# Kernel tuning notes

Measured on AMD Instinct MI355X. Metric: run time of the kernel, lower is better.

The kernel has to match this reference:

```python
import jax, jax.numpy as jnp
import numpy as np

B, N, E = 128, 2048, 32768   # events, nodes per history graph, temporal edges per graph
C, TC, H = 4, 4, 2           # channels, time_channels, heads (hardcoded in source)
DH = C // H
L = 2                        # num_layers


def setup_inputs() -> dict:
    key = jax.random.key(0)
    ks = jax.random.split(key, 16)
    return {
        "x": jax.random.normal(ks[0], (B, N, C), jnp.float32),
        "edge_index": jax.random.randint(ks[1], (B, 2, E), 0, N),
        "edge_time": jax.random.uniform(ks[2], (B, E), jnp.float32),
        "timestamp": jax.random.uniform(ks[3], (B,), jnp.float32),
        "src_index": jax.random.randint(ks[4], (B,), 0, N),
        "dst_index": jax.random.randint(ks[5], (B,), 0, N),
        "time_w": jax.random.normal(ks[6], (TC,), jnp.float32),
        "time_b": jax.random.normal(ks[7], (TC,), jnp.float32),
        "Wq": jax.random.normal(ks[8], (L, C, C), jnp.float32) / np.sqrt(C).astype(np.float32),
        "Wk": jax.random.normal(ks[9], (L, C + TC, C), jnp.float32) / np.sqrt(C + TC).astype(np.float32),
        "Wv": jax.random.normal(ks[10], (L, C + TC, C), jnp.float32) / np.sqrt(C + TC).astype(np.float32),
        "Wo": jax.random.normal(ks[11], (L, C, C), jnp.float32) / np.sqrt(C).astype(np.float32),
        "bo": jnp.zeros((L, C), jnp.float32),
        "W_lin": jax.random.normal(ks[12], (2 * C + TC, 2), jnp.float32) / np.sqrt(2 * C + TC).astype(np.float32),
        "b_lin": jnp.zeros((2,), jnp.float32),
    }


def _time_enc(t, w, b):
    # TimeEncoder: cos(t * w + b)  (Bochner-style functional time encoding)
    return jnp.cos(t[..., None] * w + b)


def _encode(x, src, dst, phi, Wq, Wk, Wv, Wo, bo):
    # seg id per edge: (batch, dst node) -> flat segment for segment softmax
    seg = (jnp.arange(B, dtype=dst.dtype)[:, None] * N + dst).reshape(-1)  # [B*E]
    h = x
    for l in range(L):
        h_src = jnp.take_along_axis(h, src[:, :, None], axis=1)            # [B,E,C] gather source feats
        msg = jnp.concatenate([h_src, phi], axis=-1)                       # [B,E,C+TC]
        q = (h @ Wq[l]).reshape(B, N, C)                                   # [B,N,C]
        k = (msg @ Wk[l]).reshape(B, E, H, DH)
        v = (msg @ Wv[l]).reshape(B, E, H, DH)
        q_e = jnp.take_along_axis(q, dst[:, :, None], axis=1).reshape(B, E, H, DH)
        logits = (q_e * k).sum(-1) / np.float32(np.sqrt(DH))               # [B,E,H]
        lf = logits.reshape(B * E, H)
        m = jax.ops.segment_max(lf, seg, num_segments=B * N)               # stable softmax max
        p = jnp.exp(lf - m[seg])
        s = jax.ops.segment_sum(p, seg, num_segments=B * N)
        agg = jax.ops.segment_sum(p[:, :, None] * v.reshape(B * E, H, DH), seg, num_segments=B * N)
        attn = (agg / jnp.where(s == 0, 1.0, s)[:, :, None]).reshape(B, N, C)
        h = jax.nn.relu(h + attn @ Wo[l] + bo[l])                          # residual + out-proj + relu
    return h


def reference(x, edge_index, edge_time, timestamp, src_index, dst_index,
              time_w, time_b, Wq, Wk, Wv, Wo, bo, W_lin, b_lin):
    src, dst = edge_index[:, 0, :], edge_index[:, 1, :]
    dt = timestamp[:, None] - edge_time                                    # [B,E] time deltas vs query time
    phi = _time_enc(dt, time_w, time_b)                                    # [B,E,TC]
    h = _encode(x, src, dst, phi, Wq, Wk, Wv, Wo, bo)                      # [B,N,C]
    bidx = jnp.arange(B)
    src_x = h[bidx, src_index]                                             # [B,C]
    dst_x = h[bidx, dst_index]                                             # [B,C]
    time_x = _time_enc(timestamp, time_w, time_b)                          # [B,TC]
    feats = jnp.concatenate([src_x, dst_x, time_x], axis=-1)               # [B,12]
    return feats @ W_lin + b_lin                                           # [B,2]
```

## Files before the change

### kernel.cpp

```cpp
#include <hip/hip_runtime.h>

namespace {

constexpr int B = 128, N = 2048, E = 32768;
constexpr int LOG2N = 11, LOG2E = 15;
constexpr int QE = E / 4;
constexpr int LOG2QE = 13;

constexpr size_t OFF_H0 = 0;
constexpr size_t OFF_H1 = 4u * 1024 * 1024;
constexpr size_t OFF_S8 = 8u * 1024 * 1024;
constexpr size_t OFF_RP = 40u * 1024 * 1024;

__global__ __launch_bounds__(1024) void sort_kernel(const int* __restrict__ edge_index,
                                                    const float* __restrict__ edge_time,
                                                    const float* __restrict__ timestamp,
                                                    int2* __restrict__ sorted8,
                                                    int* __restrict__ row_ptr) {
  __shared__ int  cnt[N];
  __shared__ int  wsum[16];
  __shared__ int2 rec[QE];
  int blk = blockIdx.x, b = blk >> 2, q = blk & 3, t = threadIdx.x;

  cnt[t] = 0; cnt[t + 1024] = 0;
  __syncthreads();

  const int* src_arr = edge_index + (((size_t)(2 * b)) << LOG2E) + q * QE;
  const int* dst_arr = edge_index + (((size_t)(2 * b + 1)) << LOG2E) + q * QE;
  const float* et    = edge_time + (((size_t)b) << LOG2E) + q * QE;
  float ts = timestamp[b];

  int srcv[8], dstv[8]; float dtv[8];
#pragma unroll
  for (int k = 0; k < 8; ++k) {
    int e = t + k * 1024;
    srcv[k] = src_arr[e];
    dstv[k] = dst_arr[e];
    dtv[k]  = ts - et[e];
  }

#pragma unroll
  for (int k = 0; k < 8; ++k) atomicAdd(&cnt[dstv[k]], 1);
  __syncthreads();

  int i0 = 2 * t, i1 = 2 * t + 1;
  int l0 = cnt[i0], l1 = cnt[i1];
  int sum = l0 + l1;
  int lane = t & 63, wid = t >> 6;
  int incl = sum;
#pragma unroll
  for (int d = 1; d < 64; d <<= 1) {
    int v = __shfl_up(incl, d, 64);
    if (lane >= d) incl += v;
  }
  if (lane == 63) wsum[wid] = incl;
  __syncthreads();
  if (t < 16) {
    int v = wsum[t];
    int inc = v;
#pragma unroll
    for (int d = 1; d < 16; d <<= 1) {
      int u = __shfl_up(inc, d, 16);
      if (t >= d) inc += u;
    }
    wsum[t] = inc - v;
  }
  __syncthreads();
  int run = wsum[wid] + (incl - sum);
  int run2 = run + l0;
  int* rp = row_ptr + (size_t)blk * (N + 1);
  rp[i0] = run;
  rp[i1] = run2;
  if (t == 1023) rp[N] = QE;
  cnt[i0] = run;
  cnt[i1] = run2;
  __syncthreads();

#pragma unroll
  for (int k = 0; k < 8; ++k) {
    int pos = atomicAdd(&cnt[dstv[k]], 1);
    rec[pos] = make_int2(srcv[k], __float_as_int(dtv[k]));
  }
  __syncthreads();

  const int4* rec4 = (const int4*)rec;
  int4* out4 = (int4*)(sorted8 + (((size_t)blk) << LOG2QE));
#pragma unroll
  for (int i = t; i < QE / 2; i += 1024) out4[i] = rec4[i];
}

__global__ __launch_bounds__(1024) void layer_kernel(const float4* __restrict__ h_in,
                                                     float4* __restrict__ h_out,
                                                     const int* __restrict__ row_ptr,
                                                     const int2* __restrict__ sorted8,
                                                     const float* __restrict__ tw,
                                                     const float* __restrict__ tb,
                                                     const float* __restrict__ Wq,
                                                     const float* __restrict__ Wk,
                                                     const float* __restrict__ Wv,
                                                     const float* __restrict__ Wo,
                                                     const float* __restrict__ bo) {
  __shared__ float4 lh[N];
  int blk = blockIdx.x, b = blk >> 1, half = blk & 1, t = threadIdx.x;

  const float4* hb = h_in + (((size_t)b) << LOG2N);
  lh[t] = hb[t];
  lh[t + 1024] = hb[t + 1024];

  constexpr float INV2PI = 0.15915494309189535f;
  constexpr float QSCALE = 0.70710678118654752f * 1.4426950408889634f;
  float twf2[4], tbf2[4], wq[16], wkh[16], wkp[16], wvh[16], wvp[16];
#pragma unroll
  for (int j = 0; j < 4; j++) { twf2[j] = tw[j] * INV2PI; tbf2[j] = tb[j] * INV2PI; }
#pragma unroll
  for (int j = 0; j < 16; j++) wq[j] = Wq[j];
#pragma unroll
  for (int j = 0; j < 16; j++) { wkh[j] = Wk[j]; wkp[j] = Wk[16 + j]; }
#pragma unroll
  for (int j = 0; j < 16; j++) { wvh[j] = Wv[j]; wvp[j] = Wv[16 + j]; }
  __syncthreads();

  int n = half * 1024 + t;
  {
    float4 hn = lh[n];
    float q0 = (hn.x * wq[0] + hn.y * wq[4] + hn.z * wq[8]  + hn.w * wq[12]) * QSCALE;
    float q1 = (hn.x * wq[1] + hn.y * wq[5] + hn.z * wq[9]  + hn.w * wq[13]) * QSCALE;
    float q2 = (hn.x * wq[2] + hn.y * wq[6] + hn.z * wq[10] + hn.w * wq[14]) * QSCALE;
    float q3 = (hn.x * wq[3] + hn.y * wq[7] + hn.z * wq[11] + hn.w * wq[15]) * QSCALE;
#pragma unroll
    for (int i = 0; i < 4; i++) {
      wq[i]      = q0 * wkh[i * 4 + 0] + q1 * wkh[i * 4 + 1];
      wq[4 + i]  = q2 * wkh[i * 4 + 2] + q3 * wkh[i * 4 + 3];
      wq[8 + i]  = q0 * wkp[i * 4 + 0] + q1 * wkp[i * 4 + 1];
      wq[12 + i] = q2 * wkp[i * 4 + 2] + q3 * wkp[i * 4 + 3];
    }
  }

  int stage = 0, addr, rem, total;
  int b1, b2, b3, c1, c2, c3;
  {
    const int* rp0 = row_ptr + (size_t)(b * 4 + 0) * (N + 1);
    const int* rp1 = row_ptr + (size_t)(b * 4 + 1) * (N + 1);
    const int* rp2 = row_ptr + (size_t)(b * 4 + 2) * (N + 1);
    const int* rp3 = row_ptr + (size_t)(b * 4 + 3) * (N + 1);
    int s0 = rp0[n], e0 = rp0[n + 1];
    int s1 = rp1[n], e1 = rp1[n + 1];
    int s2 = rp2[n], e2 = rp2[n + 1];
    int s3 = rp3[n], e3 = rp3[n + 1];
    int c0 = e0 - s0; c1 = e1 - s1; c2 = e2 - s2; c3 = e3 - s3;
    total = c0 + c1 + c2 + c3;
    addr = ((b * 4 + 0) << LOG2QE) + s0; rem = c0;
    b1 = ((b * 4 + 1) << LOG2QE) + s1;
    b2 = ((b * 4 + 2) << LOG2QE) + s2;
    b3 = ((b * 4 + 3) << LOG2QE) + s3;
    while (rem <= 0 && stage < 3) {
      ++stage;
      addr = (stage == 1) ? b1 : (stage == 2) ? b2 : b3;
      rem  = (stage == 1) ? c1 : (stage == 2) ? c2 : c3;
    }
  }

#define ADV() do { ++addr; --rem;                                   \
    while (rem <= 0 && stage < 3) { ++stage;                        \
      addr = (stage == 1) ? b1 : (stage == 2) ? b2 : b3;            \
      rem  = (stage == 1) ? c1 : (stage == 2) ? c2 : c3; } } while (0)
#define HW_COS(d, s) asm("v_cos_f32 %0, %1" : "=v"(d) : "v"(s))
#define HW_EXP2(d, s) asm("v_exp_f32 %0, %1" : "=v"(d) : "v"(s))

  float s0v = 0.f, s1v = 0.f, a00 = 0.f, a01 = 0.f, a10 = 0.f, a11 = 0.f;

  int2 r0 = sorted8[addr]; ADV();
  int2 r1 = sorted8[addr]; ADV();
  int2 r2 = sorted8[addr]; ADV();
  int2 r3 = sorted8[addr]; ADV();
  float4 hsN = lh[r0.x & (N - 1)];

  for (int it = 0; it < total; ++it) {
    int2 cur = r0;
    float4 hs = hsN;
    r0 = r1; r1 = r2; r2 = r3;
    r3 = sorted8[addr]; ADV();
    hsN = lh[r0.x & (N - 1)];

    float dt = __int_as_float(cur.y);
    float ph0, ph1, ph2, ph3;
    HW_COS(ph0, dt * twf2[0] + tbf2[0]);
    HW_COS(ph1, dt * twf2[1] + tbf2[1]);
    HW_COS(ph2, dt * twf2[2] + tbf2[2]);
    HW_COS(ph3, dt * twf2[3] + tbf2[3]);

    float l0 = hs.x * wq[0] + hs.y * wq[1] + hs.z * wq[2]  + hs.w * wq[3]
             + ph0 * wq[8] + ph1 * wq[9] + ph2 * wq[10] + ph3 * wq[11];
    float l1 = hs.x * wq[4] + hs.y * wq[5] + hs.z * wq[6]  + hs.w * wq[7]
             + ph0 * wq[12] + ph1 * wq[13] + ph2 * wq[14] + ph3 * wq[15];

    float p0, p1;
    HW_EXP2(p0, l0);
    HW_EXP2(p1, l1);

    float v0 = hs.x * wvh[0] + hs.y * wvh[4] + hs.z * wvh[8]  + hs.w * wvh[12]
             + ph0 * wvp[0] + ph1 * wvp[4] + ph2 * wvp[8]  + ph3 * wvp[12];
    float v1 = hs.x * wvh[1] + hs.y * wvh[5] + hs.z * wvh[9]  + hs.w * wvh[13]
             + ph0 * wvp[1] + ph1 * wvp[5] + ph2 * wvp[9]  + ph3 * wvp[13];
    float v2 = hs.x * wvh[2] + hs.y * wvh[6] + hs.z * wvh[10] + hs.w * wvh[14]
             + ph0 * wvp[2] + ph1 * wvp[6] + ph2 * wvp[10] + ph3 * wvp[14];
    float v3 = hs.x * wvh[3] + hs.y * wvh[7] + hs.z * wvh[11] + hs.w * wvh[15]
             + ph0 * wvp[3] + ph1 * wvp[7] + ph2 * wvp[11] + ph3 * wvp[15];

    s0v += p0; a00 += p0 * v0; a01 += p0 * v1;
    s1v += p1; a10 += p1 * v2; a11 += p1 * v3;
  }
#undef ADV
#undef HW_COS
#undef HW_EXP2

  float den0 = (s0v == 0.f) ? 1.f : s0v;
  float den1 = (s1v == 0.f) ? 1.f : s1v;
  float at0 = a00 / den0, at1 = a01 / den0, at2 = a10 / den1, at3 = a11 / den1;

  float wof[16], bof[4];
#pragma unroll
  for (int j = 0; j < 16; j++) wof[j] = Wo[j];
#pragma unroll
  for (int j = 0; j < 4; j++) bof[j] = bo[j];

  float4 hn = lh[n];
  float o0 = bof[0] + at0 * wof[0] + at1 * wof[4] + at2 * wof[8]  + at3 * wof[12];
  float o1 = bof[1] + at0 * wof[1] + at1 * wof[5] + at2 * wof[9]  + at3 * wof[13];
  float o2 = bof[2] + at0 * wof[2] + at1 * wof[6] + at2 * wof[10] + at3 * wof[14];
  float o3 = bof[3] + at0 * wof[3] + at1 * wof[7] + at2 * wof[11] + at3 * wof[15];
  h_out[(((size_t)b) << LOG2N) + n] =
      make_float4(fmaxf(hn.x + o0, 0.f), fmaxf(hn.y + o1, 0.f),
                  fmaxf(hn.z + o2, 0.f), fmaxf(hn.w + o3, 0.f));
}

__global__ void final_kernel(const float4* __restrict__ h,
                             const int* __restrict__ src_index, const int* __restrict__ dst_index,
                             const float* __restrict__ timestamp,
                             const float* __restrict__ tw,
                             const float* __restrict__ tb,
                             const float* __restrict__ W_lin,
                             const float* __restrict__ b_lin,
                             float* __restrict__ out) {
  int b = threadIdx.x;
  if (b >= B) return;
  float4 sx = h[(((size_t)b) << LOG2N) + src_index[b]];
  float4 dx = h[(((size_t)b) << LOG2N) + dst_index[b]];
  float ts = timestamp[b];
  float f[12];
  f[0] = sx.x; f[1] = sx.y; f[2] = sx.z; f[3] = sx.w;
  f[4] = dx.x; f[5] = dx.y; f[6] = dx.z; f[7] = dx.w;
#pragma unroll
  for (int j = 0; j < 4; j++) f[8 + j] = __cosf(ts * tw[j] + tb[j]);
#pragma unroll
  for (int c = 0; c < 2; c++) {
    float o = b_lin[c];
#pragma unroll
    for (int j = 0; j < 12; j++) o += f[j] * W_lin[j * 2 + c];
    out[b * 2 + c] = o;
  }
}

}

extern "C" void kernel_launch(void* const* d_in, const int* in_sizes, int n_in,
                              void* d_out, int out_size, void* d_ws, size_t ws_size,
                              hipStream_t stream) {
  (void)in_sizes; (void)n_in; (void)out_size; (void)ws_size;
  const float* x         = (const float*)d_in[0];
  const int*   edge_idx  = (const int*)d_in[1];
  const float* edge_time = (const float*)d_in[2];
  const float* timestamp = (const float*)d_in[3];
  const int*   src_index = (const int*)d_in[4];
  const int*   dst_index = (const int*)d_in[5];
  const float* time_w    = (const float*)d_in[6];
  const float* time_b    = (const float*)d_in[7];
  const float* Wq        = (const float*)d_in[8];
  const float* Wk        = (const float*)d_in[9];
  const float* Wv        = (const float*)d_in[10];
  const float* Wo        = (const float*)d_in[11];
  const float* bo        = (const float*)d_in[12];
  const float* W_lin     = (const float*)d_in[13];
  const float* b_lin     = (const float*)d_in[14];

  char* ws = (char*)d_ws;
  float4* h0      = (float4*)(ws + OFF_H0);
  float4* h1      = (float4*)(ws + OFF_H1);
  int2*   sorted8 = (int2*)(ws + OFF_S8);
  int*    row_ptr = (int*)(ws + OFF_RP);

  sort_kernel<<<4 * B, 1024, 0, stream>>>(edge_idx, edge_time, timestamp, sorted8, row_ptr);

  layer_kernel<<<2 * B, 1024, 0, stream>>>((const float4*)x, h1, row_ptr, sorted8,
                                           time_w, time_b,
                                           Wq + 0 * 16, Wk + 0 * 32, Wv + 0 * 32,
                                           Wo + 0 * 16, bo + 0 * 4);
  layer_kernel<<<2 * B, 1024, 0, stream>>>(h1, h0, row_ptr, sorted8,
                                           time_w, time_b,
                                           Wq + 1 * 16, Wk + 1 * 32, Wv + 1 * 32,
                                           Wo + 1 * 16, bo + 1 * 4);

  final_kernel<<<1, 128, 0, stream>>>(h0, src_index, dst_index, timestamp, time_w, time_b,
                                      W_lin, b_lin, (float*)d_out);
}
```

Measured before the change: 166.7 us.

## Fuse sort, both layers and final head into one cooperative persistent kernel

Replaces four kernel launches with a single cooperative kernel of 256 blocks that sort, run both attention layers and compute the final linear head, separated by grid-wide syncs. Each block sorts two edge quarters, then reuses its row-pointer loads across both layers. Blocks are mapped so a batch's blocks share an XCD for L2 locality. It removes launch gaps and redundant row_ptr reads, but adds grid-sync overhead and halves sort parallelism, since each block now does two quarters serially.

```diff
diff --git a/kernel.cpp b/kernel.cpp
--- a/kernel.cpp
+++ b/kernel.cpp
@@ -1,4 +1,7 @@
 #include <hip/hip_runtime.h>
+#include <hip/hip_cooperative_groups.h>
+
+namespace cg = cooperative_groups;
 
 namespace {
 
@@ -12,101 +15,50 @@
 constexpr size_t OFF_S8 = 8u * 1024 * 1024;
 constexpr size_t OFF_RP = 40u * 1024 * 1024;
 
-__global__ __launch_bounds__(1024) void sort_kernel(const int* __restrict__ edge_index,
-                                                    const float* __restrict__ edge_time,
-                                                    const float* __restrict__ timestamp,
-                                                    int2* __restrict__ sorted8,
-                                                    int* __restrict__ row_ptr) {
-  __shared__ int  cnt[N];
-  __shared__ int  wsum[16];
-  __shared__ int2 rec[QE];
-  int blk = blockIdx.x, b = blk >> 2, q = blk & 3, t = threadIdx.x;
-
-  cnt[t] = 0; cnt[t + 1024] = 0;
-  __syncthreads();
-
-  const int* src_arr = edge_index + (((size_t)(2 * b)) << LOG2E) + q * QE;
-  const int* dst_arr = edge_index + (((size_t)(2 * b + 1)) << LOG2E) + q * QE;
-  const float* et    = edge_time + (((size_t)b) << LOG2E) + q * QE;
-  float ts = timestamp[b];
-
-  int srcv[8], dstv[8]; float dtv[8];
-#pragma unroll
-  for (int k = 0; k < 8; ++k) {
-    int e = t + k * 1024;
-    srcv[k] = src_arr[e];
-    dstv[k] = dst_arr[e];
-    dtv[k]  = ts - et[e];
-  }
-
-#pragma unroll
-  for (int k = 0; k < 8; ++k) atomicAdd(&cnt[dstv[k]], 1);
-  __syncthreads();
-
-  int i0 = 2 * t, i1 = 2 * t + 1;
-  int l0 = cnt[i0], l1 = cnt[i1];
-  int sum = l0 + l1;
-  int lane = t & 63, wid = t >> 6;
-  int incl = sum;
-#pragma unroll
-  for (int d = 1; d < 64; d <<= 1) {
-    int v = __shfl_up(incl, d, 64);
-    if (lane >= d) incl += v;
-  }
-  if (lane == 63) wsum[wid] = incl;
-  __syncthreads();
-  if (t < 16) {
-    int v = wsum[t];
-    int inc = v;
-#pragma unroll
-    for (int d = 1; d < 16; d <<= 1) {
-      int u = __shfl_up(inc, d, 16);
-      if (t >= d) inc += u;
-    }
-    wsum[t] = inc - v;
-  }
-  __syncthreads();
-  int run = wsum[wid] + (incl - sum);
-  int run2 = run + l0;
-  int* rp = row_ptr + (size_t)blk * (N + 1);
-  rp[i0] = run;
-  rp[i1] = run2;
-  if (t == 1023) rp[N] = QE;
-  cnt[i0] = run;
-  cnt[i1] = run2;
-  __syncthreads();
-
-#pragma unroll
-  for (int k = 0; k < 8; ++k) {
-    int pos = atomicAdd(&cnt[dstv[k]], 1);
-    rec[pos] = make_int2(srcv[k], __float_as_int(dtv[k]));
-  }
-  __syncthreads();
-
-  const int4* rec4 = (const int4*)rec;
-  int4* out4 = (int4*)(sorted8 + (((size_t)blk) << LOG2QE));
-#pragma unroll
-  for (int i = t; i < QE / 2; i += 1024) out4[i] = rec4[i];
-}
-
-__global__ __launch_bounds__(1024) void layer_kernel(const float4* __restrict__ h_in,
-                                                     float4* __restrict__ h_out,
-                                                     const int* __restrict__ row_ptr,
-                                                     const int2* __restrict__ sorted8,
-                                                     const float* __restrict__ tw,
-                                                     const float* __restrict__ tb,
-                                                     const float* __restrict__ Wq,
-                                                     const float* __restrict__ Wk,
-                                                     const float* __restrict__ Wv,
-                                                     const float* __restrict__ Wo,
-                                                     const float* __restrict__ bo) {
-  __shared__ float4 lh[N];
-  int blk = blockIdx.x, b = blk >> 1, half = blk & 1, t = threadIdx.x;
-
+struct Params {
+  const float4* x;
+  const int*    edge_index;
+  const float*  edge_time;
+  const float*  timestamp;
+  const int*    src_index;
+  const int*    dst_index;
+  const float*  tw;
+  const float*  tb;
+  const float*  Wq;
+  const float*  Wk;
+  const float*  Wv;
+  const float*  Wo;
+  const float*  bo;
+  const float*  W_lin;
+  const float*  b_lin;
+  float4* h0;
+  float4* h1;
+  int2*   sorted8;
+  int*    row_ptr;
+  float*  out;
+};
+
+__device__ __forceinline__ float hw_cos(float s)  { float d; asm("v_cos_f32 %0, %1" : "=v"(d) : "v"(s)); return d; }
+__device__ __forceinline__ float hw_exp2(float s) { float d; asm("v_exp_f32 %0, %1" : "=v"(d) : "v"(s)); return d; }
+
+struct SortS { int cnt[N]; int wsum[16]; int2 rec[QE]; };
+
+__device__ __forceinline__ void layer_phase(
+    const Params& P, int b, int n, int t, int l,
+    const float4* __restrict__ h_in, float4* __restrict__ h_out, float4* lh,
+    int s0, int s1, int s2, int s3, int c0, int c1, int c2, int c3) {
   const float4* hb = h_in + (((size_t)b) << LOG2N);
   lh[t] = hb[t];
   lh[t + 1024] = hb[t + 1024];
 
+  const float* tw = P.tw;
+  const float* tb = P.tb;
+  const float* Wq = P.Wq + l * 16;
+  const float* Wk = P.Wk + l * 32;
+  const float* Wv = P.Wv + l * 32;
+  const float* Wo = P.Wo + l * 16;
+  const float* bo = P.bo + l * 4;
+
   constexpr float INV2PI = 0.15915494309189535f;
   constexpr float QSCALE = 0.70710678118654752f * 1.4426950408889634f;
   float twf2[4], tbf2[4], wq[16], wkh[16], wkp[16], wvh[16], wvp[16];
@@ -120,7 +72,6 @@
   for (int j = 0; j < 16; j++) { wvh[j] = Wv[j]; wvp[j] = Wv[16 + j]; }
   __syncthreads();
 
-  int n = half * 1024 + t;
   {
     float4 hn = lh[n];
     float q0 = (hn.x * wq[0] + hn.y * wq[4] + hn.z * wq[8]  + hn.w * wq[12]) * QSCALE;
@@ -136,67 +87,52 @@
     }
   }
 
-  int stage = 0, addr, rem, total;
-  int b1, b2, b3, c1, c2, c3;
-  {
-    const int* rp0 = row_ptr + (size_t)(b * 4 + 0) * (N + 1);
-    const int* rp1 = row_ptr + (size_t)(b * 4 + 1) * (N + 1);
-    const int* rp2 = row_ptr + (size_t)(b * 4 + 2) * (N + 1);
-    const int* rp3 = row_ptr + (size_t)(b * 4 + 3) * (N + 1);
-    int s0 = rp0[n], e0 = rp0[n + 1];
-    int s1 = rp1[n], e1 = rp1[n + 1];
-    int s2 = rp2[n], e2 = rp2[n + 1];
-    int s3 = rp3[n], e3 = rp3[n + 1];
-    int c0 = e0 - s0; c1 = e1 - s1; c2 = e2 - s2; c3 = e3 - s3;
-    total = c0 + c1 + c2 + c3;
-    addr = ((b * 4 + 0) << LOG2QE) + s0; rem = c0;
-    b1 = ((b * 4 + 1) << LOG2QE) + s1;
-    b2 = ((b * 4 + 2) << LOG2QE) + s2;
-    b3 = ((b * 4 + 3) << LOG2QE) + s3;
-    while (rem <= 0 && stage < 3) {
-      ++stage;
-      addr = (stage == 1) ? b1 : (stage == 2) ? b2 : b3;
-      rem  = (stage == 1) ? c1 : (stage == 2) ? c2 : c3;
-    }
+  int stage = 0;
+  int total = c0 + c1 + c2 + c3;
+  int addr = ((b * 4 + 0) << LOG2QE) + s0, rem = c0;
+  int b1 = ((b * 4 + 1) << LOG2QE) + s1;
+  int b2 = ((b * 4 + 2) << LOG2QE) + s2;
+  int b3 = ((b * 4 + 3) << LOG2QE) + s3;
+  while (rem <= 0 && stage < 3) {
+    ++stage;
+    addr = (stage == 1) ? b1 : (stage == 2) ? b2 : b3;
+    rem  = (stage == 1) ? c1 : (stage == 2) ? c2 : c3;
   }
 
 #define ADV() do { ++addr; --rem;                                   \
     while (rem <= 0 && stage < 3) { ++stage;                        \
       addr = (stage == 1) ? b1 : (stage == 2) ? b2 : b3;            \
       rem  = (stage == 1) ? c1 : (stage == 2) ? c2 : c3; } } while (0)
-#define HW_COS(d, s) asm("v_cos_f32 %0, %1" : "=v"(d) : "v"(s))
-#define HW_EXP2(d, s) asm("v_exp_f32 %0, %1" : "=v"(d) : "v"(s))
 
   float s0v = 0.f, s1v = 0.f, a00 = 0.f, a01 = 0.f, a10 = 0.f, a11 = 0.f;
 
-  int2 r0 = sorted8[addr]; ADV();
-  int2 r1 = sorted8[addr]; ADV();
-  int2 r2 = sorted8[addr]; ADV();
-  int2 r3 = sorted8[addr]; ADV();
+  const int2* __restrict__ srt = P.sorted8;
+  int2 r0 = srt[addr]; ADV();
+  int2 r1 = srt[addr]; ADV();
+  int2 r2 = srt[addr]; ADV();
+  int2 r3 = srt[addr]; ADV();
   float4 hsN = lh[r0.x & (N - 1)];
 
   for (int it = 0; it < total; ++it) {
     int2 cur = r0;
     float4 hs = hsN;
     r0 = r1; r1 = r2; r2 = r3;
-    r3 = sorted8[addr]; ADV();
+    r3 = srt[addr]; ADV();
     hsN = lh[r0.x & (N - 1)];
 
     float dt = __int_as_float(cur.y);
-    float ph0, ph1, ph2, ph3;
-    HW_COS(ph0, dt * twf2[0] + tbf2[0]);
-    HW_COS(ph1, dt * twf2[1] + tbf2[1]);
-    HW_COS(ph2, dt * twf2[2] + tbf2[2]);
-    HW_COS(ph3, dt * twf2[3] + tbf2[3]);
+    float ph0 = hw_cos(dt * twf2[0] + tbf2[0]);
+    float ph1 = hw_cos(dt * twf2[1] + tbf2[1]);
+    float ph2 = hw_cos(dt * twf2[2] + tbf2[2]);
+    float ph3 = hw_cos(dt * twf2[3] + tbf2[3]);
 
     float l0 = hs.x * wq[0] + hs.y * wq[1] + hs.z * wq[2]  + hs.w * wq[3]
              + ph0 * wq[8] + ph1 * wq[9] + ph2 * wq[10] + ph3 * wq[11];
     float l1 = hs.x * wq[4] + hs.y * wq[5] + hs.z * wq[6]  + hs.w * wq[7]
              + ph0 * wq[12] + ph1 * wq[13] + ph2 * wq[14] + ph3 * wq[15];
 
-    float p0, p1;
-    HW_EXP2(p0, l0);
-    HW_EXP2(p1, l1);
+    float p0 = hw_exp2(l0);
+    float p1 = hw_exp2(l1);
 
     float v0 = hs.x * wvh[0] + hs.y * wvh[4] + hs.z * wvh[8]  + hs.w * wvh[12]
              + ph0 * wvp[0] + ph1 * wvp[4] + ph2 * wvp[8]  + ph3 * wvp[12];
@@ -211,8 +147,6 @@
     s1v += p1; a10 += p1 * v2; a11 += p1 * v3;
   }
 #undef ADV
-#undef HW_COS
-#undef HW_EXP2
 
   float den0 = (s0v == 0.f) ? 1.f : s0v;
   float den1 = (s1v == 0.f) ? 1.f : s1v;
@@ -234,30 +168,127 @@
                   fmaxf(hn.z + o2, 0.f), fmaxf(hn.w + o3, 0.f));
 }
 
-__global__ void final_kernel(const float4* __restrict__ h,
-                             const int* __restrict__ src_index, const int* __restrict__ dst_index,
-                             const float* __restrict__ timestamp,
-                             const float* __restrict__ tw,
-                             const float* __restrict__ tb,
-                             const float* __restrict__ W_lin,
-                             const float* __restrict__ b_lin,
-                             float* __restrict__ out) {
-  int b = threadIdx.x;
-  if (b >= B) return;
-  float4 sx = h[(((size_t)b) << LOG2N) + src_index[b]];
-  float4 dx = h[(((size_t)b) << LOG2N) + dst_index[b]];
-  float ts = timestamp[b];
-  float f[12];
-  f[0] = sx.x; f[1] = sx.y; f[2] = sx.z; f[3] = sx.w;
-  f[4] = dx.x; f[5] = dx.y; f[6] = dx.z; f[7] = dx.w;
-#pragma unroll
-  for (int j = 0; j < 4; j++) f[8 + j] = __cosf(ts * tw[j] + tb[j]);
-#pragma unroll
-  for (int c = 0; c < 2; c++) {
-    float o = b_lin[c];
-#pragma unroll
-    for (int j = 0; j < 12; j++) o += f[j] * W_lin[j * 2 + c];
-    out[b * 2 + c] = o;
+__global__ __launch_bounds__(1024) void fused_kernel(Params P) {
+  __shared__ __align__(16) char smem[sizeof(SortS)];
+  int p = blockIdx.x, t = threadIdx.x;
+  int xcd = p & 7, slot = p >> 3;
+  int b = xcd * 16 + (slot >> 1);
+  int half = slot & 1;
+
+  {
+    SortS& S = *reinterpret_cast<SortS*>(smem);
+    float ts = P.timestamp[b];
+    for (int qi = 0; qi < 2; ++qi) {
+      int q = 2 * half + qi;
+      int blk = b * 4 + q;
+      S.cnt[t] = 0; S.cnt[t + 1024] = 0;
+      __syncthreads();
+
+      const int* src_arr = P.edge_index + (((size_t)(2 * b)) << LOG2E) + q * QE;
+      const int* dst_arr = P.edge_index + (((size_t)(2 * b + 1)) << LOG2E) + q * QE;
+      const float* et    = P.edge_time + (((size_t)b) << LOG2E) + q * QE;
+
+      int srcv[8], dstv[8]; float dtv[8];
+#pragma unroll
+      for (int k = 0; k < 8; ++k) {
+        int e = t + k * 1024;
+        srcv[k] = src_arr[e];
+        dstv[k] = dst_arr[e];
+        dtv[k]  = ts - et[e];
+      }
+#pragma unroll
+      for (int k = 0; k < 8; ++k) atomicAdd(&S.cnt[dstv[k]], 1);
+      __syncthreads();
+
+      int i0 = 2 * t, i1 = 2 * t + 1;
+      int l0 = S.cnt[i0], l1 = S.cnt[i1];
+      int sum = l0 + l1;
+      int lane = t & 63, wid = t >> 6;
+      int incl = sum;
+#pragma unroll
+      for (int d = 1; d < 64; d <<= 1) {
+        int v = __shfl_up(incl, d, 64);
+        if (lane >= d) incl += v;
+      }
+      if (lane == 63) S.wsum[wid] = incl;
+      __syncthreads();
+      if (t < 16) {
+        int v = S.wsum[t];
+        int inc = v;
+#pragma unroll
+        for (int d = 1; d < 16; d <<= 1) {
+          int u = __shfl_up(inc, d, 16);
+          if (t >= d) inc += u;
+        }
+        S.wsum[t] = inc - v;
+      }
+      __syncthreads();
+      int run = S.wsum[wid] + (incl - sum);
+      int run2 = run + l0;
+      int* rp = P.row_ptr + (size_t)blk * (N + 1);
+      rp[i0] = run;
+      rp[i1] = run2;
+      if (t == 1023) rp[N] = QE;
+      S.cnt[i0] = run;
+      S.cnt[i1] = run2;
+      __syncthreads();
+
+#pragma unroll
+      for (int k = 0; k < 8; ++k) {
+        int pos = atomicAdd(&S.cnt[dstv[k]], 1);
+        S.rec[pos] = make_int2(srcv[k], __float_as_int(dtv[k]));
+      }
+      __syncthreads();
+
+      const int4* rec4 = (const int4*)S.rec;
+      int4* out4 = (int4*)(P.sorted8 + (((size_t)blk) << LOG2QE));
+      for (int i = t; i < QE / 2; i += 1024) out4[i] = rec4[i];
+      __syncthreads();
+    }
+  }
+  __threadfence();
+  cg::this_grid().sync();
+
+  int n = half * 1024 + t;
+  int s0, s1, s2, s3, c0, c1, c2, c3;
+  {
+    const int* rp0 = P.row_ptr + (size_t)(b * 4 + 0) * (N + 1);
+    const int* rp1 = P.row_ptr + (size_t)(b * 4 + 1) * (N + 1);
+    const int* rp2 = P.row_ptr + (size_t)(b * 4 + 2) * (N + 1);
+    const int* rp3 = P.row_ptr + (size_t)(b * 4 + 3) * (N + 1);
+    s0 = rp0[n]; c0 = rp0[n + 1] - s0;
+    s1 = rp1[n]; c1 = rp1[n + 1] - s1;
+    s2 = rp2[n]; c2 = rp2[n + 1] - s2;
+    s3 = rp3[n]; c3 = rp3[n + 1] - s3;
+  }
+
+  float4* lh = reinterpret_cast<float4*>(smem);
+
+  layer_phase(P, b, n, t, 0, P.x, P.h1, lh, s0, s1, s2, s3, c0, c1, c2, c3);
+  __threadfence();
+  cg::this_grid().sync();
+
+  layer_phase(P, b, n, t, 1, P.h1, P.h0, lh, s0, s1, s2, s3, c0, c1, c2, c3);
+  __threadfence();
+  cg::this_grid().sync();
+
+  if (p == 0 && t < B) {
+    int bb = t;
+    float4 sx = P.h0[(((size_t)bb) << LOG2N) + P.src_index[bb]];
+    float4 dx = P.h0[(((size_t)bb) << LOG2N) + P.dst_index[bb]];
+    float ts = P.timestamp[bb];
+    float f[12];
+    f[0] = sx.x; f[1] = sx.y; f[2] = sx.z; f[3] = sx.w;
+    f[4] = dx.x; f[5] = dx.y; f[6] = dx.z; f[7] = dx.w;
+#pragma unroll
+    for (int j = 0; j < 4; j++) f[8 + j] = __cosf(ts * P.tw[j] + P.tb[j]);
+#pragma unroll
+    for (int c = 0; c < 2; c++) {
+      float o = P.b_lin[c];
+#pragma unroll
+      for (int j = 0; j < 12; j++) o += f[j] * P.W_lin[j * 2 + c];
+      P.out[bb * 2 + c] = o;
+    }
   }
 }
 
@@ -267,39 +298,31 @@
                               void* d_out, int out_size, void* d_ws, size_t ws_size,
                               hipStream_t stream) {
   (void)in_sizes; (void)n_in; (void)out_size; (void)ws_size;
-  const float* x         = (const float*)d_in[0];
-  const int*   edge_idx  = (const int*)d_in[1];
-  const float* edge_time = (const float*)d_in[2];
-  const float* timestamp = (const float*)d_in[3];
-  const int*   src_index = (const int*)d_in[4];
-  const int*   dst_index = (const int*)d_in[5];
-  const float* time_w    = (const float*)d_in[6];
-  const float* time_b    = (const float*)d_in[7];
-  const float* Wq        = (const float*)d_in[8];
-  const float* Wk        = (const float*)d_in[9];
-  const float* Wv        = (const float*)d_in[10];
-  const float* Wo        = (const float*)d_in[11];
-  const float* bo        = (const float*)d_in[12];
-  const float* W_lin     = (const float*)d_in[13];
-  const float* b_lin     = (const float*)d_in[14];
-
   char* ws = (char*)d_ws;
-  float4* h0      = (float4*)(ws + OFF_H0);
-  float4* h1      = (float4*)(ws + OFF_H1);
-  int2*   sorted8 = (int2*)(ws + OFF_S8);
-  int*    row_ptr = (int*)(ws + OFF_RP);
-
-  sort_kernel<<<4 * B, 1024, 0, stream>>>(edge_idx, edge_time, timestamp, sorted8, row_ptr);
-
-  layer_kernel<<<2 * B, 1024, 0, stream>>>((const float4*)x, h1, row_ptr, sorted8,
-                                           time_w, time_b,
-                                           Wq + 0 * 16, Wk + 0 * 32, Wv + 0 * 32,
-                                           Wo + 0 * 16, bo + 0 * 4);
-  layer_kernel<<<2 * B, 1024, 0, stream>>>(h1, h0, row_ptr, sorted8,
-                                           time_w, time_b,
-                                           Wq + 1 * 16, Wk + 1 * 32, Wv + 1 * 32,
-                                           Wo + 1 * 16, bo + 1 * 4);
-
-  final_kernel<<<1, 128, 0, stream>>>(h0, src_index, dst_index, timestamp, time_w, time_b,
-                                      W_lin, b_lin, (float*)d_out);
+
+  Params hp;
+  hp.x          = (const float4*)d_in[0];
+  hp.edge_index = (const int*)d_in[1];
+  hp.edge_time  = (const float*)d_in[2];
+  hp.timestamp  = (const float*)d_in[3];
+  hp.src_index  = (const int*)d_in[4];
+  hp.dst_index  = (const int*)d_in[5];
+  hp.tw         = (const float*)d_in[6];
+  hp.tb         = (const float*)d_in[7];
+  hp.Wq         = (const float*)d_in[8];
+  hp.Wk         = (const float*)d_in[9];
+  hp.Wv         = (const float*)d_in[10];
+  hp.Wo         = (const float*)d_in[11];
+  hp.bo         = (const float*)d_in[12];
+  hp.W_lin      = (const float*)d_in[13];
+  hp.b_lin      = (const float*)d_in[14];
+  hp.h0         = (float4*)(ws + OFF_H0);
+  hp.h1         = (float4*)(ws + OFF_H1);
+  hp.sorted8    = (int2*)(ws + OFF_S8);
+  hp.row_ptr    = (int*)(ws + OFF_RP);
+  hp.out        = (float*)d_out;
+
+  void* kargs[] = { (void*)&hp };
+  hipLaunchCooperativeKernel((void*)fused_kernel, dim3(2 * B), dim3(1024),
+                             kargs, 0, stream);
 }
```

Measured after the change: 522.3 us. 3.13x slower.

## Switch to edge-parallel segmented scan aggregation with partial sums per layer

Applied to the files above, without the earlier changes.

Replaces the node-parallel CSR walk, where each thread loops over its node's edges with divergent trip counts, with an edge-parallel pass. Each thread handles one dst-sorted edge, reduces runs of equal destination with a wave segmented scan, and adds run totals into shared-memory accumulators with atomics. Layer outputs are no longer materialised in full: layer 0 writes partial softmax sums, layer 1 rebuilds h1 from them on load, and layer 2 is only evaluated at the src/dst query nodes in the final kernel. This removes the row_ptr traffic and the load imbalance, at the cost of extra shuffles and LDS atomics per edge and recomputing q per edge.

```diff
diff --git a/kernel.cpp b/kernel.cpp
--- a/kernel.cpp
+++ b/kernel.cpp
@@ -7,16 +7,17 @@
 constexpr int QE = E / 4;
 constexpr int LOG2QE = 13;
 
-constexpr size_t OFF_H0 = 0;
-constexpr size_t OFF_H1 = 4u * 1024 * 1024;
-constexpr size_t OFF_S8 = 8u * 1024 * 1024;
-constexpr size_t OFF_RP = 40u * 1024 * 1024;
+constexpr size_t OFF_S8 = 0;
+constexpr size_t OFF_P1 = 32u * 1024 * 1024;
+constexpr size_t OFF_O2 = OFF_P1 + 12u * 1024 * 1024;
+
+__device__ __forceinline__ float hw_cos(float s)  { float d; asm("v_cos_f32 %0, %1" : "=v"(d) : "v"(s)); return d; }
+__device__ __forceinline__ float hw_exp2(float s) { float d; asm("v_exp_f32 %0, %1" : "=v"(d) : "v"(s)); return d; }
 
 __global__ __launch_bounds__(1024) void sort_kernel(const int* __restrict__ edge_index,
                                                     const float* __restrict__ edge_time,
                                                     const float* __restrict__ timestamp,
-                                                    int2* __restrict__ sorted8,
-                                                    int* __restrict__ row_ptr) {
+                                                    int2* __restrict__ sorted8) {
   __shared__ int  cnt[N];
   __shared__ int  wsum[16];
   __shared__ int2 rec[QE];
@@ -38,7 +39,6 @@
     dstv[k] = dst_arr[e];
     dtv[k]  = ts - et[e];
   }
-
 #pragma unroll
   for (int k = 0; k < 8; ++k) atomicAdd(&cnt[dstv[k]], 1);
   __syncthreads();
@@ -67,136 +67,121 @@
   }
   __syncthreads();
   int run = wsum[wid] + (incl - sum);
-  int run2 = run + l0;
-  int* rp = row_ptr + (size_t)blk * (N + 1);
-  rp[i0] = run;
-  rp[i1] = run2;
-  if (t == 1023) rp[N] = QE;
   cnt[i0] = run;
-  cnt[i1] = run2;
+  cnt[i1] = run + l0;
   __syncthreads();
 
 #pragma unroll
   for (int k = 0; k < 8; ++k) {
     int pos = atomicAdd(&cnt[dstv[k]], 1);
-    rec[pos] = make_int2(srcv[k], __float_as_int(dtv[k]));
+    rec[pos] = make_int2(srcv[k] | (dstv[k] << 16), __float_as_int(dtv[k]));
   }
   __syncthreads();
 
   const int4* rec4 = (const int4*)rec;
   int4* out4 = (int4*)(sorted8 + (((size_t)blk) << LOG2QE));
-#pragma unroll
   for (int i = t; i < QE / 2; i += 1024) out4[i] = rec4[i];
 }
 
-__global__ __launch_bounds__(1024) void layer_kernel(const float4* __restrict__ h_in,
-                                                     float4* __restrict__ h_out,
-                                                     const int* __restrict__ row_ptr,
-                                                     const int2* __restrict__ sorted8,
-                                                     const float* __restrict__ tw,
-                                                     const float* __restrict__ tb,
-                                                     const float* __restrict__ Wq,
-                                                     const float* __restrict__ Wk,
-                                                     const float* __restrict__ Wv,
-                                                     const float* __restrict__ Wo,
-                                                     const float* __restrict__ bo) {
+template <int MODE>
+__global__ __launch_bounds__(1024, 4) void layerE_kernel(
+    const float4* __restrict__ x, const int2* __restrict__ sorted8,
+    const float* __restrict__ part1, float* __restrict__ part1out,
+    float* __restrict__ out2,
+    const int* __restrict__ src_index, const int* __restrict__ dst_index,
+    const float* __restrict__ tw, const float* __restrict__ tb,
+    const float* __restrict__ Wq, const float* __restrict__ Wk,
+    const float* __restrict__ Wv, const float* __restrict__ WoP,
+    const float* __restrict__ boP) {
   __shared__ float4 lh[N];
+  __shared__ float  accS[6 * N];
   int blk = blockIdx.x, b = blk >> 1, half = blk & 1, t = threadIdx.x;
-
-  const float4* hb = h_in + (((size_t)b) << LOG2N);
-  lh[t] = hb[t];
-  lh[t + 1024] = hb[t + 1024];
+  int lane = t & 63;
 
   constexpr float INV2PI = 0.15915494309189535f;
   constexpr float QSCALE = 0.70710678118654752f * 1.4426950408889634f;
-  float twf2[4], tbf2[4], wq[16], wkh[16], wkp[16], wvh[16], wvp[16];
+  float twf2[4], tbf2[4], wqc[16], wkh[16], wkp[16], wvh[16], wvp[16];
 #pragma unroll
   for (int j = 0; j < 4; j++) { twf2[j] = tw[j] * INV2PI; tbf2[j] = tb[j] * INV2PI; }
 #pragma unroll
-  for (int j = 0; j < 16; j++) wq[j] = Wq[j];
+  for (int j = 0; j < 16; j++) wqc[j] = Wq[j] * QSCALE;
 #pragma unroll
   for (int j = 0; j < 16; j++) { wkh[j] = Wk[j]; wkp[j] = Wk[16 + j]; }
 #pragma unroll
   for (int j = 0; j < 16; j++) { wvh[j] = Wv[j]; wvp[j] = Wv[16 + j]; }
-  __syncthreads();
-
-  int n = half * 1024 + t;
+
+  if constexpr (MODE == 0) {
+    const float4* hb = x + (((size_t)b) << LOG2N);
+    lh[t] = hb[t];
+    lh[t + 1024] = hb[t + 1024];
+  } else {
+    const float* p1 = part1 + ((size_t)(b * 2)) * 6 * N;
+#pragma unroll
+    for (int nn = 0; nn < 2; ++nn) {
+      int n = t + nn * 1024;
+      float sarr[6];
+#pragma unroll
+      for (int j = 0; j < 6; j++) sarr[j] = p1[j * N + n] + p1[6 * N + j * N + n];
+      float den0 = (sarr[0] == 0.f) ? 1.f : sarr[0];
+      float den1 = (sarr[1] == 0.f) ? 1.f : sarr[1];
+      float at0 = sarr[2] / den0, at1 = sarr[3] / den0;
+      float at2 = sarr[4] / den1, at3 = sarr[5] / den1;
+      float4 xb = x[(((size_t)b) << LOG2N) + n];
+      float o0 = boP[0] + at0 * WoP[0] + at1 * WoP[4] + at2 * WoP[8]  + at3 * WoP[12];
+      float o1 = boP[1] + at0 * WoP[1] + at1 * WoP[5] + at2 * WoP[9]  + at3 * WoP[13];
+      float o2 = boP[2] + at0 * WoP[2] + at1 * WoP[6] + at2 * WoP[10] + at3 * WoP[14];
+      float o3 = boP[3] + at0 * WoP[3] + at1 * WoP[7] + at2 * WoP[11] + at3 * WoP[15];
+      lh[n] = make_float4(fmaxf(xb.x + o0, 0.f), fmaxf(xb.y + o1, 0.f),
+                          fmaxf(xb.z + o2, 0.f), fmaxf(xb.w + o3, 0.f));
+    }
+  }
   {
-    float4 hn = lh[n];
-    float q0 = (hn.x * wq[0] + hn.y * wq[4] + hn.z * wq[8]  + hn.w * wq[12]) * QSCALE;
-    float q1 = (hn.x * wq[1] + hn.y * wq[5] + hn.z * wq[9]  + hn.w * wq[13]) * QSCALE;
-    float q2 = (hn.x * wq[2] + hn.y * wq[6] + hn.z * wq[10] + hn.w * wq[14]) * QSCALE;
-    float q3 = (hn.x * wq[3] + hn.y * wq[7] + hn.z * wq[11] + hn.w * wq[15]) * QSCALE;
-#pragma unroll
-    for (int i = 0; i < 4; i++) {
-      wq[i]      = q0 * wkh[i * 4 + 0] + q1 * wkh[i * 4 + 1];
-      wq[4 + i]  = q2 * wkh[i * 4 + 2] + q3 * wkh[i * 4 + 3];
-      wq[8 + i]  = q0 * wkp[i * 4 + 0] + q1 * wkp[i * 4 + 1];
-      wq[12 + i] = q2 * wkp[i * 4 + 2] + q3 * wkp[i * 4 + 3];
-    }
-  }
-
-  int stage = 0, addr, rem, total;
-  int b1, b2, b3, c1, c2, c3;
-  {
-    const int* rp0 = row_ptr + (size_t)(b * 4 + 0) * (N + 1);
-    const int* rp1 = row_ptr + (size_t)(b * 4 + 1) * (N + 1);
-    const int* rp2 = row_ptr + (size_t)(b * 4 + 2) * (N + 1);
-    const int* rp3 = row_ptr + (size_t)(b * 4 + 3) * (N + 1);
-    int s0 = rp0[n], e0 = rp0[n + 1];
-    int s1 = rp1[n], e1 = rp1[n + 1];
-    int s2 = rp2[n], e2 = rp2[n + 1];
-    int s3 = rp3[n], e3 = rp3[n + 1];
-    int c0 = e0 - s0; c1 = e1 - s1; c2 = e2 - s2; c3 = e3 - s3;
-    total = c0 + c1 + c2 + c3;
-    addr = ((b * 4 + 0) << LOG2QE) + s0; rem = c0;
-    b1 = ((b * 4 + 1) << LOG2QE) + s1;
-    b2 = ((b * 4 + 2) << LOG2QE) + s2;
-    b3 = ((b * 4 + 3) << LOG2QE) + s3;
-    while (rem <= 0 && stage < 3) {
-      ++stage;
-      addr = (stage == 1) ? b1 : (stage == 2) ? b2 : b3;
-      rem  = (stage == 1) ? c1 : (stage == 2) ? c2 : c3;
-    }
-  }
-
-#define ADV() do { ++addr; --rem;                                   \
-    while (rem <= 0 && stage < 3) { ++stage;                        \
-      addr = (stage == 1) ? b1 : (stage == 2) ? b2 : b3;            \
-      rem  = (stage == 1) ? c1 : (stage == 2) ? c2 : c3; } } while (0)
-#define HW_COS(d, s) asm("v_cos_f32 %0, %1" : "=v"(d) : "v"(s))
-#define HW_EXP2(d, s) asm("v_exp_f32 %0, %1" : "=v"(d) : "v"(s))
-
-  float s0v = 0.f, s1v = 0.f, a00 = 0.f, a01 = 0.f, a10 = 0.f, a11 = 0.f;
-
-  int2 r0 = sorted8[addr]; ADV();
-  int2 r1 = sorted8[addr]; ADV();
-  int2 r2 = sorted8[addr]; ADV();
-  int2 r3 = sorted8[addr]; ADV();
-  float4 hsN = lh[r0.x & (N - 1)];
-
-  for (int it = 0; it < total; ++it) {
-    int2 cur = r0;
-    float4 hs = hsN;
-    r0 = r1; r1 = r2; r2 = r3;
-    r3 = sorted8[addr]; ADV();
-    hsN = lh[r0.x & (N - 1)];
-
-    float dt = __int_as_float(cur.y);
-    float ph0, ph1, ph2, ph3;
-    HW_COS(ph0, dt * twf2[0] + tbf2[0]);
-    HW_COS(ph1, dt * twf2[1] + tbf2[1]);
-    HW_COS(ph2, dt * twf2[2] + tbf2[2]);
-    HW_COS(ph3, dt * twf2[3] + tbf2[3]);
-
-    float l0 = hs.x * wq[0] + hs.y * wq[1] + hs.z * wq[2]  + hs.w * wq[3]
-             + ph0 * wq[8] + ph1 * wq[9] + ph2 * wq[10] + ph3 * wq[11];
-    float l1 = hs.x * wq[4] + hs.y * wq[5] + hs.z * wq[6]  + hs.w * wq[7]
-             + ph0 * wq[12] + ph1 * wq[13] + ph2 * wq[14] + ph3 * wq[15];
-
-    float p0, p1;
-    HW_EXP2(p0, l0);
-    HW_EXP2(p1, l1);
+    float4* a4 = (float4*)accS;
+    float4 z = make_float4(0.f, 0.f, 0.f, 0.f);
+    a4[t] = z; a4[t + 1024] = z; a4[t + 2048] = z;
+  }
+  __syncthreads();
+
+  const int2* __restrict__ srt = sorted8 + (((size_t)(b * 4 + half * 2)) << LOG2QE);
+
+#define SEGSCAN(y) do { float u_;                                   \
+    u_ = __shfl_up(y, 1, 64);  if (lane - 1  >= hd_i) y += u_;      \
+    u_ = __shfl_up(y, 2, 64);  if (lane - 2  >= hd_i) y += u_;      \
+    u_ = __shfl_up(y, 4, 64);  if (lane - 4  >= hd_i) y += u_;      \
+    u_ = __shfl_up(y, 8, 64);  if (lane - 8  >= hd_i) y += u_;      \
+    u_ = __shfl_up(y, 16, 64); if (lane - 16 >= hd_i) y += u_;      \
+    u_ = __shfl_up(y, 32, 64); if (lane - 32 >= hd_i) y += u_;      \
+  } while (0)
+
+  for (int k = 0; k < 16; ++k) {
+    int2 rc = srt[k * 1024 + t];
+    int sidx = rc.x & 0xffff;
+    int didx = ((unsigned)rc.x) >> 16;
+    float dt = __int_as_float(rc.y);
+    float4 hs = lh[sidx];
+    float4 hd = lh[didx];
+
+    float ph0 = hw_cos(dt * twf2[0] + tbf2[0]);
+    float ph1 = hw_cos(dt * twf2[1] + tbf2[1]);
+    float ph2 = hw_cos(dt * twf2[2] + tbf2[2]);
+    float ph3 = hw_cos(dt * twf2[3] + tbf2[3]);
+
+    float q0 = hd.x * wqc[0] + hd.y * wqc[4] + hd.z * wqc[8]  + hd.w * wqc[12];
+    float q1 = hd.x * wqc[1] + hd.y * wqc[5] + hd.z * wqc[9]  + hd.w * wqc[13];
+    float q2 = hd.x * wqc[2] + hd.y * wqc[6] + hd.z * wqc[10] + hd.w * wqc[14];
+    float q3 = hd.x * wqc[3] + hd.y * wqc[7] + hd.z * wqc[11] + hd.w * wqc[15];
+
+    float k0 = hs.x * wkh[0] + hs.y * wkh[4] + hs.z * wkh[8]  + hs.w * wkh[12]
+             + ph0 * wkp[0] + ph1 * wkp[4] + ph2 * wkp[8]  + ph3 * wkp[12];
+    float k1 = hs.x * wkh[1] + hs.y * wkh[5] + hs.z * wkh[9]  + hs.w * wkh[13]
+             + ph0 * wkp[1] + ph1 * wkp[5] + ph2 * wkp[9]  + ph3 * wkp[13];
+    float k2 = hs.x * wkh[2] + hs.y * wkh[6] + hs.z * wkh[10] + hs.w * wkh[14]
+             + ph0 * wkp[2] + ph1 * wkp[6] + ph2 * wkp[10] + ph3 * wkp[14];
+    float k3 = hs.x * wkh[3] + hs.y * wkh[7] + hs.z * wkh[11] + hs.w * wkh[15]
+             + ph0 * wkp[3] + ph1 * wkp[7] + ph2 * wkp[11] + ph3 * wkp[15];
+
+    float p0 = hw_exp2(q0 * k0 + q1 * k1);
+    float p1 = hw_exp2(q2 * k2 + q3 * k3);
 
     float v0 = hs.x * wvh[0] + hs.y * wvh[4] + hs.z * wvh[8]  + hs.w * wvh[12]
              + ph0 * wvp[0] + ph1 * wvp[4] + ph2 * wvp[8]  + ph3 * wvp[12];
@@ -207,49 +192,96 @@
     float v3 = hs.x * wvh[3] + hs.y * wvh[7] + hs.z * wvh[11] + hs.w * wvh[15]
              + ph0 * wvp[3] + ph1 * wvp[7] + ph2 * wvp[11] + ph3 * wvp[15];
 
-    s0v += p0; a00 += p0 * v0; a01 += p0 * v1;
-    s1v += p1; a10 += p1 * v2; a11 += p1 * v3;
-  }
-#undef ADV
-#undef HW_COS
-#undef HW_EXP2
-
-  float den0 = (s0v == 0.f) ? 1.f : s0v;
-  float den1 = (s1v == 0.f) ? 1.f : s1v;
-  float at0 = a00 / den0, at1 = a01 / den0, at2 = a10 / den1, at3 = a11 / den1;
-
-  float wof[16], bof[4];
-#pragma unroll
-  for (int j = 0; j < 16; j++) wof[j] = Wo[j];
-#pragma unroll
-  for (int j = 0; j < 4; j++) bof[j] = bo[j];
-
-  float4 hn = lh[n];
-  float o0 = bof[0] + at0 * wof[0] + at1 * wof[4] + at2 * wof[8]  + at3 * wof[12];
-  float o1 = bof[1] + at0 * wof[1] + at1 * wof[5] + at2 * wof[9]  + at3 * wof[13];
-  float o2 = bof[2] + at0 * wof[2] + at1 * wof[6] + at2 * wof[10] + at3 * wof[14];
-  float o3 = bof[3] + at0 * wof[3] + at1 * wof[7] + at2 * wof[11] + at3 * wof[15];
-  h_out[(((size_t)b) << LOG2N) + n] =
-      make_float4(fmaxf(hn.x + o0, 0.f), fmaxf(hn.y + o1, 0.f),
-                  fmaxf(hn.z + o2, 0.f), fmaxf(hn.w + o3, 0.f));
-}
-
-__global__ void final_kernel(const float4* __restrict__ h,
+    float y0 = p0, y1 = p1;
+    float y2 = p0 * v0, y3 = p0 * v1, y4 = p1 * v2, y5 = p1 * v3;
+
+    int dprev = __shfl_up(didx, 1, 64);
+    int hd_i = (lane == 0 || didx != dprev) ? lane : 0;
+#pragma unroll
+    for (int d = 1; d < 64; d <<= 1) {
+      int u = __shfl_up(hd_i, d, 64);
+      if (lane >= d) hd_i = max(hd_i, u);
+    }
+    SEGSCAN(y0); SEGSCAN(y1); SEGSCAN(y2); SEGSCAN(y3); SEGSCAN(y4); SEGSCAN(y5);
+
+    int dnext = __shfl_down(didx, 1, 64);
+    bool tail = (lane == 63) || (didx != dnext);
+    if (tail) {
+      atomicAdd(&accS[0 * N + didx], y0);
+      atomicAdd(&accS[1 * N + didx], y1);
+      atomicAdd(&accS[2 * N + didx], y2);
+      atomicAdd(&accS[3 * N + didx], y3);
+      atomicAdd(&accS[4 * N + didx], y4);
+      atomicAdd(&accS[5 * N + didx], y5);
+    }
+  }
+#undef SEGSCAN
+
+  __syncthreads();
+
+  if constexpr (MODE == 0) {
+    float* po = part1out + ((size_t)(b * 2 + half)) * 6 * N;
+#pragma unroll
+    for (int j = 0; j < 6; j++) {
+      po[j * N + t] = accS[j * N + t];
+      po[j * N + t + 1024] = accS[j * N + t + 1024];
+    }
+  } else {
+    if (t < 12) {
+      int slot = t / 6, j = t % 6;
+      int node = (slot == 0) ? src_index[b] : dst_index[b];
+      out2[(((size_t)(b * 2 + half)) * 2 + slot) * 6 + j] = accS[j * N + node];
+    }
+  }
+}
+
+__global__ void final_kernel(const float4* __restrict__ x,
+                             const float* __restrict__ part1,
+                             const float* __restrict__ out2,
                              const int* __restrict__ src_index, const int* __restrict__ dst_index,
                              const float* __restrict__ timestamp,
-                             const float* __restrict__ tw,
-                             const float* __restrict__ tb,
-                             const float* __restrict__ W_lin,
-                             const float* __restrict__ b_lin,
+                             const float* __restrict__ tw, const float* __restrict__ tb,
+                             const float* __restrict__ Wo, const float* __restrict__ bo,
+                             const float* __restrict__ W_lin, const float* __restrict__ b_lin,
                              float* __restrict__ out) {
   int b = threadIdx.x;
   if (b >= B) return;
-  float4 sx = h[(((size_t)b) << LOG2N) + src_index[b]];
-  float4 dx = h[(((size_t)b) << LOG2N) + dst_index[b]];
+  int nodes[2] = { src_index[b], dst_index[b] };
   float ts = timestamp[b];
+  const float* p1 = part1 + ((size_t)(b * 2)) * 6 * N;
+  float h2v[2][4];
+#pragma unroll
+  for (int slot = 0; slot < 2; ++slot) {
+    int n = nodes[slot];
+    float sarr[6];
+#pragma unroll
+    for (int j = 0; j < 6; j++) sarr[j] = p1[j * N + n] + p1[6 * N + j * N + n];
+    float den0 = (sarr[0] == 0.f) ? 1.f : sarr[0];
+    float den1 = (sarr[1] == 0.f) ? 1.f : sarr[1];
+    float at0 = sarr[2] / den0, at1 = sarr[3] / den0;
+    float at2 = sarr[4] / den1, at3 = sarr[5] / den1;
+    float4 xb = x[(((size_t)b) << LOG2N) + n];
+    float h10 = fmaxf(xb.x + bo[0] + at0 * Wo[0] + at1 * Wo[4] + at2 * Wo[8]  + at3 * Wo[12], 0.f);
+    float h11 = fmaxf(xb.y + bo[1] + at0 * Wo[1] + at1 * Wo[5] + at2 * Wo[9]  + at3 * Wo[13], 0.f);
+    float h12 = fmaxf(xb.z + bo[2] + at0 * Wo[2] + at1 * Wo[6] + at2 * Wo[10] + at3 * Wo[14], 0.f);
+    float h13 = fmaxf(xb.w + bo[3] + at0 * Wo[3] + at1 * Wo[7] + at2 * Wo[11] + at3 * Wo[15], 0.f);
+    float t2[6];
+#pragma unroll
+    for (int j = 0; j < 6; j++)
+      t2[j] = out2[(((size_t)(b * 2 + 0)) * 2 + slot) * 6 + j]
+            + out2[(((size_t)(b * 2 + 1)) * 2 + slot) * 6 + j];
+    float d20 = (t2[0] == 0.f) ? 1.f : t2[0];
+    float d21 = (t2[1] == 0.f) ? 1.f : t2[1];
+    float b0 = t2[2] / d20, b1 = t2[3] / d20, b2 = t2[4] / d21, b3 = t2[5] / d21;
+    const float* Wo1 = Wo + 16; const float* bo1 = bo + 4;
+    h2v[slot][0] = fmaxf(h10 + bo1[0] + b0 * Wo1[0] + b1 * Wo1[4] + b2 * Wo1[8]  + b3 * Wo1[12], 0.f);
+    h2v[slot][1] = fmaxf(h11 + bo1[1] + b0 * Wo1[1] + b1 * Wo1[5] + b2 * Wo1[9]  + b3 * Wo1[13], 0.f);
+    h2v[slot][2] = fmaxf(h12 + bo1[2] + b0 * Wo1[2] + b1 * Wo1[6] + b2 * Wo1[10] + b3 * Wo1[14], 0.f);
+    h2v[slot][3] = fmaxf(h13 + bo1[3] + b0 * Wo1[3] + b1 * Wo1[7] + b2 * Wo1[11] + b3 * Wo1[15], 0.f);
+  }
   float f[12];
-  f[0] = sx.x; f[1] = sx.y; f[2] = sx.z; f[3] = sx.w;
-  f[4] = dx.x; f[5] = dx.y; f[6] = dx.z; f[7] = dx.w;
+#pragma unroll
+  for (int j = 0; j < 4; j++) { f[j] = h2v[0][j]; f[4 + j] = h2v[1][j]; }
 #pragma unroll
   for (int j = 0; j < 4; j++) f[8 + j] = __cosf(ts * tw[j] + tb[j]);
 #pragma unroll
@@ -284,22 +316,21 @@
   const float* b_lin     = (const float*)d_in[14];
 
   char* ws = (char*)d_ws;
-  float4* h0      = (float4*)(ws + OFF_H0);
-  float4* h1      = (float4*)(ws + OFF_H1);
-  int2*   sorted8 = (int2*)(ws + OFF_S8);
-  int*    row_ptr = (int*)(ws + OFF_RP);
-
-  sort_kernel<<<4 * B, 1024, 0, stream>>>(edge_idx, edge_time, timestamp, sorted8, row_ptr);
-
-  layer_kernel<<<2 * B, 1024, 0, stream>>>((const float4*)x, h1, row_ptr, sorted8,
-                                           time_w, time_b,
-                                           Wq + 0 * 16, Wk + 0 * 32, Wv + 0 * 32,
-                                           Wo + 0 * 16, bo + 0 * 4);
-  layer_kernel<<<2 * B, 1024, 0, stream>>>(h1, h0, row_ptr, sorted8,
-                                           time_w, time_b,
-                                           Wq + 1 * 16, Wk + 1 * 32, Wv + 1 * 32,
-                                           Wo + 1 * 16, bo + 1 * 4);
-
-  final_kernel<<<1, 128, 0, stream>>>(h0, src_index, dst_index, timestamp, time_w, time_b,
-                                      W_lin, b_lin, (float*)d_out);
-}
+  int2*  sorted8 = (int2*)(ws + OFF_S8);
+  float* part1   = (float*)(ws + OFF_P1);
+  float* out2    = (float*)(ws + OFF_O2);
+
+  sort_kernel<<<4 * B, 1024, 0, stream>>>(edge_idx, edge_time, timestamp, sorted8);
+
+  layerE_kernel<0><<<2 * B, 1024, 0, stream>>>(
+      (const float4*)x, sorted8, nullptr, part1, nullptr, src_index, dst_index,
+      time_w, time_b, Wq + 0, Wk + 0, Wv + 0, nullptr, nullptr);
+
+  layerE_kernel<1><<<2 * B, 1024, 0, stream>>>(
+      (const float4*)x, sorted8, part1, nullptr, out2, src_index, dst_index,
+      time_w, time_b, Wq + 16, Wk + 32, Wv + 32, Wo + 0, bo + 0);
+
+  final_kernel<<<1, 128, 0, stream>>>(
+      (const float4*)x, part1, out2, src_index, dst_index, timestamp,
+      time_w, time_b, Wo, bo, W_lin, b_lin, (float*)d_out);
+}
```

Measured after the change: 268.7 us. +61.2%, slower.

## Sort nodes by in-degree so each wavefront processes similar-degree nodes

Applied to the files above, without the earlier changes.

Adds a per-graph kernel that computes each node's total in-degree across the four edge quarters, buckets the nodes by degree (capped at 63) with a shared-memory histogram, and writes a node permutation. The layer kernels then map threads to nodes through this permutation, so lanes in a wavefront walk similar-length edge lists and spend less time idle from divergence. The cost is an extra launch, an indirect node index, and scattered rather than contiguous writes of node outputs. Because the permutation is a valid reordering, results should be unchanged.

```diff
diff --git a/kernel.cpp b/kernel.cpp
--- a/kernel.cpp
+++ b/kernel.cpp
@@ -11,6 +11,7 @@
 constexpr size_t OFF_H1 = 4u * 1024 * 1024;
 constexpr size_t OFF_S8 = 8u * 1024 * 1024;
 constexpr size_t OFF_RP = 40u * 1024 * 1024;
+constexpr size_t OFF_PM = 45u * 1024 * 1024;
 
 __global__ __launch_bounds__(1024) void sort_kernel(const int* __restrict__ edge_index,
                                                     const float* __restrict__ edge_time,
@@ -89,10 +90,47 @@
   for (int i = t; i < QE / 2; i += 1024) out4[i] = rec4[i];
 }
 
+__global__ __launch_bounds__(256) void perm_kernel(const int* __restrict__ row_ptr,
+                                                   int* __restrict__ perm) {
+  __shared__ int hist[64];
+  __shared__ int base[64];
+  int b = blockIdx.x, t = threadIdx.x;
+  if (t < 64) hist[t] = 0;
+  __syncthreads();
+  int deg[8];
+#pragma unroll
+  for (int k = 0; k < 8; ++k) {
+    int n = t + k * 256;
+    int d = 0;
+#pragma unroll
+    for (int q = 0; q < 4; ++q) {
+      const int* rp = row_ptr + (size_t)(b * 4 + q) * (N + 1);
+      d += rp[n + 1] - rp[n];
+    }
+    deg[k] = min(d, 63);
+    atomicAdd(&hist[deg[k]], 1);
+  }
+  __syncthreads();
+  if (t == 0) {
+    int run = 0;
+    for (int i = 0; i < 64; ++i) { base[i] = run; run += hist[i]; }
+  }
+  __syncthreads();
+  if (t < 64) hist[t] = 0;
+  __syncthreads();
+#pragma unroll
+  for (int k = 0; k < 8; ++k) {
+    int n = t + k * 256;
+    int r = base[deg[k]] + atomicAdd(&hist[deg[k]], 1);
+    perm[(size_t)b * N + r] = n;
+  }
+}
+
 __global__ __launch_bounds__(1024) void layer_kernel(const float4* __restrict__ h_in,
                                                      float4* __restrict__ h_out,
                                                      const int* __restrict__ row_ptr,
                                                      const int2* __restrict__ sorted8,
+                                                     const int* __restrict__ perm,
                                                      const float* __restrict__ tw,
                                                      const float* __restrict__ tb,
                                                      const float* __restrict__ Wq,
@@ -120,7 +158,7 @@
   for (int j = 0; j < 16; j++) { wvh[j] = Wv[j]; wvp[j] = Wv[16 + j]; }
   __syncthreads();
 
-  int n = half * 1024 + t;
+  int n = perm[(size_t)b * N + half * 1024 + t];
   {
     float4 hn = lh[n];
     float q0 = (hn.x * wq[0] + hn.y * wq[4] + hn.z * wq[8]  + hn.w * wq[12]) * QSCALE;
@@ -288,14 +326,17 @@
   float4* h1      = (float4*)(ws + OFF_H1);
   int2*   sorted8 = (int2*)(ws + OFF_S8);
   int*    row_ptr = (int*)(ws + OFF_RP);
+  int*    perm    = (int*)(ws + OFF_PM);
 
   sort_kernel<<<4 * B, 1024, 0, stream>>>(edge_idx, edge_time, timestamp, sorted8, row_ptr);
 
-  layer_kernel<<<2 * B, 1024, 0, stream>>>((const float4*)x, h1, row_ptr, sorted8,
+  perm_kernel<<<B, 256, 0, stream>>>(row_ptr, perm);
+
+  layer_kernel<<<2 * B, 1024, 0, stream>>>((const float4*)x, h1, row_ptr, sorted8, perm,
                                            time_w, time_b,
                                            Wq + 0 * 16, Wk + 0 * 32, Wv + 0 * 32,
                                            Wo + 0 * 16, bo + 0 * 4);
-  layer_kernel<<<2 * B, 1024, 0, stream>>>(h1, h0, row_ptr, sorted8,
+  layer_kernel<<<2 * B, 1024, 0, stream>>>(h1, h0, row_ptr, sorted8, perm,
                                            time_w, time_b,
                                            Wq + 1 * 16, Wk + 1 * 32, Wv + 1 * 32,
                                            Wo + 1 * 16, bo + 1 * 4);
```

After: 193.2 us. 1.16x slower.
